# Performance work log

Hardware: AMD Instinct MI355X
Metric: run time of the kernel (lower is better)

The kernel has to match this reference:

```python
import jax, jax.numpy as jnp
import numpy as np

N = 50000
E = 800000
IN_DIM = 256
HID = 64
HEADS = 4
OUT_DIM = 40
NEG_SLOPE = 0.2


def _gatv2_conv(x, src, dst, Wl, bl, Wr, br, att, bias, concat):
    """PyG GATv2Conv (share_weights=False, eval mode, no attn dropout).
    src -> message source nodes, dst -> target nodes (softmax over dst)."""
    H, C = att.shape
    n = x.shape[0]
    xl = (x @ Wl + bl).reshape(n, H, C)  # source/message transform (lin_l)
    xr = (x @ Wr + br).reshape(n, H, C)  # target transform (lin_r)
    # per-edge logits: [E, H]
    s = xl[src] + xr[dst]                                  # [E,H,C]
    e = jnp.einsum('ehc,hc->eh', jax.nn.leaky_relu(s, NEG_SLOPE), att)
    # segment softmax over incoming edges of each target node
    m = jax.ops.segment_max(e, dst, num_segments=n)        # [N,H]
    m = jnp.where(jnp.isfinite(m), m, 0.0)                 # empty segments
    ex = jnp.exp(e - m[dst])
    denom = jax.ops.segment_sum(ex, dst, num_segments=n)   # [N,H]
    alpha = ex / (denom[dst] + 1e-16)                      # [E,H]
    out = jax.ops.segment_sum(alpha[:, :, None] * xl[src], dst, num_segments=n)
    if concat:
        out = out.reshape(n, H * C)
    else:
        out = out.mean(axis=1)
    return out + bias


def setup_inputs() -> dict:
    key = jax.random.key(0)
    ks = jax.random.split(key, 12)
    sc = 0.05
    return {
        'x': jax.random.normal(ks[0], (N, IN_DIM), jnp.float32),
        'src': jax.random.randint(ks[1], (E,), 0, N, jnp.int32),
        'dst': jax.random.randint(ks[2], (E,), 0, N, jnp.int32),
        'Wl1': jax.random.normal(ks[3], (IN_DIM, HEADS * HID), jnp.float32) * sc,
        'bl1': jnp.zeros((HEADS * HID,), jnp.float32),
        'Wr1': jax.random.normal(ks[4], (IN_DIM, HEADS * HID), jnp.float32) * sc,
        'br1': jnp.zeros((HEADS * HID,), jnp.float32),
        'att1': jax.random.normal(ks[5], (HEADS, HID), jnp.float32) * sc,
        'bias1': jnp.zeros((HEADS * HID,), jnp.float32),
        'Wl2': jax.random.normal(ks[6], (HEADS * HID, HEADS * HID), jnp.float32) * sc,
        'bl2': jnp.zeros((HEADS * HID,), jnp.float32),
        'Wr2': jax.random.normal(ks[7], (HEADS * HID, HEADS * HID), jnp.float32) * sc,
        'br2': jnp.zeros((HEADS * HID,), jnp.float32),
        'att2': jax.random.normal(ks[8], (HEADS, HID), jnp.float32) * sc,
        'bias2': jnp.zeros((HID,), jnp.float32),
        'Wc': jax.random.normal(ks[9], (HID, OUT_DIM), jnp.float32) * sc,
        'bc': jnp.zeros((OUT_DIM,), jnp.float32),
    }


def reference(x, src, dst, Wl1, bl1, Wr1, br1, att1, bias1,
              Wl2, bl2, Wr2, br2, att2, bias2, Wc, bc):
    h = _gatv2_conv(x, src, dst, Wl1, bl1, Wr1, br1, att1, bias1, concat=True)
    h = jax.nn.relu(h)  # dropout p applied only in training; eval -> identity
    h = _gatv2_conv(h, src, dst, Wl2, bl2, Wr2, br2, att2, bias2, concat=False)
    h = jax.nn.relu(h)
    return h @ Wc + bc  # [N, OUT_DIM]
```

## Files before the change

### kernel.cpp

```cpp
#include <hip/hip_runtime.h>
#include <hip/hip_bf16.h>
#include <math.h>


#define IN_DIM 256
#define HIDHC 256
#define HID 64
#define OUT_DIM 40

using half8  = __attribute__((ext_vector_type(8))) _Float16;
using half4  = __attribute__((ext_vector_type(4))) _Float16;
using half2v = __attribute__((ext_vector_type(2))) _Float16;
using f32x4  = __attribute__((ext_vector_type(4))) float;

__device__ __forceinline__ void gload16(const void* g, void* l) {
    __builtin_amdgcn_global_load_lds(
        (const __attribute__((address_space(1))) void*)g,
        (__attribute__((address_space(3))) void*)l, 16, 0, 0);
}


__global__ void edge_hist(const int* __restrict__ dst, int* __restrict__ deg, int E) {
    int i = blockIdx.x * blockDim.x + threadIdx.x;
    if (i < E) atomicAdd(&deg[dst[i]], 1);
}

__global__ void deg_block_reduce(const int* __restrict__ deg, int* __restrict__ bsum, int n) {
    int i = blockIdx.x * 256 + threadIdx.x;
    int v = (i < n) ? deg[i] : 0;
    #pragma unroll
    for (int off = 32; off; off >>= 1) v += __shfl_xor(v, off, 64);
    __shared__ int ws[4];
    int lane = threadIdx.x & 63, wid = threadIdx.x >> 6;
    if (lane == 0) ws[wid] = v;
    __syncthreads();
    if (threadIdx.x == 0) bsum[blockIdx.x] = ws[0] + ws[1] + ws[2] + ws[3];
}

__global__ void scan_bsums(const int* __restrict__ bsum, int* __restrict__ bpre, int nb) {
    __shared__ int s[256];
    int tid = threadIdx.x;
    int orig = (tid < nb) ? bsum[tid] : 0;
    s[tid] = orig;
    __syncthreads();
    #pragma unroll
    for (int off = 1; off < 256; off <<= 1) {
        int t = (tid >= off) ? s[tid - off] : 0;
        __syncthreads();
        s[tid] += t;
        __syncthreads();
    }
    if (tid < nb) bpre[tid] = s[tid] - orig;
}

__global__ void deg_scan_apply(const int* __restrict__ deg, const int* __restrict__ bpre,
                               int* __restrict__ offsets, int* __restrict__ cursor, int n) {
    int i = blockIdx.x * 256 + threadIdx.x;
    int lane = threadIdx.x & 63, wid = threadIdx.x >> 6;
    int v = (i < n) ? deg[i] : 0;
    int inc = v;
    #pragma unroll
    for (int off = 1; off < 64; off <<= 1) {
        int t = __shfl_up(inc, off, 64);
        if (lane >= off) inc += t;
    }
    __shared__ int ws[4];
    if (lane == 63) ws[wid] = inc;
    __syncthreads();
    int add = bpre[blockIdx.x];
    for (int w = 0; w < wid; ++w) add += ws[w];
    int incl = inc + add;
    if (i < n) { offsets[i + 1] = incl; cursor[i] = incl - v; }
    if (i == 0) offsets[0] = 0;
}

__global__ void edge_scatter(const int* __restrict__ src, const int* __restrict__ dst,
                             int* __restrict__ cursor, int* __restrict__ csr_src, int E) {
    int i = blockIdx.x * blockDim.x + threadIdx.x;
    if (i < E) {
        int p = atomicAdd(&cursor[dst[i]], 1);
        csr_src[p] = src[i];
    }
}


__global__ void cvt_f16(const float* __restrict__ in, _Float16* __restrict__ out, int n4) {
    int i = blockIdx.x * blockDim.x + threadIdx.x;
    if (i >= n4) return;
    float4 v = ((const float4*)in)[i];
    half4 h = { (_Float16)v.x, (_Float16)v.y, (_Float16)v.z, (_Float16)v.w };
    ((half4*)out)[i] = h;
}

__global__ void prep_weights(const float* __restrict__ W0, const float* __restrict__ W1,
                             const float* __restrict__ W2, const float* __restrict__ W3,
                             _Float16* __restrict__ T) {
    const float* Wsel = (blockIdx.y == 0) ? W0 : (blockIdx.y == 1) ? W1
                      : (blockIdx.y == 2) ? W2 : W3;
    int k = blockIdx.x, nn = threadIdx.x;
    float v = Wsel[k * 256 + nn];
    T[(size_t)blockIdx.y * 65536 + (size_t)nn * 256 + k] = (_Float16)v;
}


__global__ __launch_bounds__(256) void gemm2_mfma(
    const _Float16* __restrict__ A,
    const _Float16* __restrict__ W0, const float* __restrict__ b0, _Float16* __restrict__ C0,
    const _Float16* __restrict__ W1, const float* __restrict__ b1, _Float16* __restrict__ C1,
    int M)
{
    __shared__ __align__(16) _Float16 sA[2][4096], sB[2][4096];

    const _Float16* W   = blockIdx.z ? W1 : W0;
    const float*    bias= blockIdx.z ? b1 : b0;
    _Float16*       C   = blockIdx.z ? C1 : C0;

    int tid = threadIdx.x;
    int bm = blockIdx.x * 128;
    int bn = blockIdx.y * 128;

    int lane = tid & 63, w = tid >> 6;
    int r = lane & 15, q = lane >> 4;
    int m0 = (w >> 1) * 64, n0 = (w & 1) * 64;

    int arow[2], brow[2], kgo[2], lds[2];
    #pragma unroll
    for (int i = 0; i < 2; ++i) {
        int g = tid + 256 * i;
        kgo[i] = (g >> 7) * 8;
        int row = g & 127;
        arow[i] = min(bm + row, M - 1);
        brow[i] = bn + row;
        lds[i] = g * 8;
    }

    f32x4 acc[4][4];
    #pragma unroll
    for (int i = 0; i < 4; ++i)
        #pragma unroll
        for (int j = 0; j < 4; ++j) acc[i][j] = (f32x4)0.f;

    #pragma unroll
    for (int i = 0; i < 2; ++i) {
        gload16(A + (size_t)arow[i] * 256 + kgo[i], &sA[0][lds[i]]);
        gload16(W + (size_t)brow[i] * 256 + kgo[i], &sB[0][lds[i]]);
    }
    __builtin_amdgcn_s_waitcnt(0);
    __syncthreads();

    #pragma unroll 1
    for (int kt = 0; kt < 8; ++kt) {
        int buf = kt & 1;
        if (kt < 7) {
            int k0 = (kt + 1) * 32;
            #pragma unroll
            for (int i = 0; i < 2; ++i) {
                gload16(A + (size_t)arow[i] * 256 + k0 + kgo[i], &sA[buf ^ 1][lds[i]]);
                gload16(W + (size_t)brow[i] * 256 + k0 + kgo[i], &sB[buf ^ 1][lds[i]]);
            }
        }
        half8 a[4], b[4];
        #pragma unroll
        for (int i = 0; i < 4; ++i) {
            a[i] = *(const half8*)(&sA[buf][(q * 128 + m0 + i * 16 + r) * 8]);
            b[i] = *(const half8*)(&sB[buf][(q * 128 + n0 + i * 16 + r) * 8]);
        }
        #pragma unroll
        for (int i = 0; i < 4; ++i)
            #pragma unroll
            for (int j = 0; j < 4; ++j)
                acc[i][j] = __builtin_amdgcn_mfma_f32_16x16x32_f16(a[i], b[j], acc[i][j], 0, 0, 0);
        __builtin_amdgcn_s_waitcnt(0);
        __syncthreads();
    }

    float bv[4];
    #pragma unroll
    for (int j = 0; j < 4; ++j) bv[j] = bias[bn + n0 + j * 16 + r];
    #pragma unroll
    for (int i = 0; i < 4; ++i) {
        #pragma unroll
        for (int reg = 0; reg < 4; ++reg) {
            int row = bm + m0 + i * 16 + q * 4 + reg;
            if (row < M) {
                #pragma unroll
                for (int j = 0; j < 4; ++j)
                    C[(size_t)row * 256 + bn + n0 + j * 16 + r] =
                        (_Float16)(acc[i][j][reg] + bv[j]);
            }
        }
    }
}


__global__ __launch_bounds__(256) void gat_node(
    const _Float16* __restrict__ xl, const _Float16* __restrict__ xr,
    const float* __restrict__ att, const float* __restrict__ bias,
    const int* __restrict__ offsets, const int* __restrict__ csr_src,
    void* __restrict__ out0, int n, int mode)
{
    int wid = threadIdx.x >> 6;
    int node = (blockIdx.x << 2) + wid;
    if (node >= n) return;
    int lane = threadIdx.x & 63;
    int H = lane >> 5;
    int p = lane & 31;

    const half2v c02 = { (_Float16)0.2f, (_Float16)0.2f };

    half8 xrh = *(const half8*)(xr + (size_t)node * HIDHC + p * 8);
    half2v xr01 = __builtin_shufflevector(xrh, xrh, 0, 1);
    half2v xr23 = __builtin_shufflevector(xrh, xrh, 2, 3);
    half2v xr45 = __builtin_shufflevector(xrh, xrh, 4, 5);
    half2v xr67 = __builtin_shufflevector(xrh, xrh, 6, 7);

    float4 af0 = *(const float4*)(att + p * 8);
    float4 af1 = *(const float4*)(att + p * 8 + 4);
    half2v at01 = { (_Float16)af0.x, (_Float16)af0.y };
    half2v at23 = { (_Float16)af0.z, (_Float16)af0.w };
    half2v at45 = { (_Float16)af1.x, (_Float16)af1.y };
    half2v at67 = { (_Float16)af1.z, (_Float16)af1.w };

    float acc[8];
    #pragma unroll
    for (int k = 0; k < 8; ++k) acc[k] = 0.f;
    float d = 0.f;

    int j0 = __builtin_amdgcn_readfirstlane(offsets[node]);
    int j1 = __builtin_amdgcn_readfirstlane(offsets[node + 1]);

    int j = j0;
    for (; j + 2 <= j1; j += 2) {
        int s0 = __builtin_amdgcn_readfirstlane(csr_src[j]);
        int s1 = __builtin_amdgcn_readfirstlane(csr_src[j + 1]);
        int s = H ? s1 : s0;
        half8 h = *(const half8*)(xl + (size_t)s * HIDHC + p * 8);
        half2v h01 = __builtin_shufflevector(h, h, 0, 1);
        half2v h23 = __builtin_shufflevector(h, h, 2, 3);
        half2v h45 = __builtin_shufflevector(h, h, 4, 5);
        half2v h67 = __builtin_shufflevector(h, h, 6, 7);
        half2v s01 = h01 + xr01, s23 = h23 + xr23, s45 = h45 + xr45, s67 = h67 + xr67;
        half2v l01 = __builtin_elementwise_max(s01, s01 * c02);
        half2v l23 = __builtin_elementwise_max(s23, s23 * c02);
        half2v l45 = __builtin_elementwise_max(s45, s45 * c02);
        half2v l67 = __builtin_elementwise_max(s67, s67 * c02);
        float e = __builtin_amdgcn_fdot2(l01, at01, 0.f, false);
        e = __builtin_amdgcn_fdot2(l23, at23, e, false);
        e = __builtin_amdgcn_fdot2(l45, at45, e, false);
        e = __builtin_amdgcn_fdot2(l67, at67, e, false);
        e += __shfl_xor(e, 1);
        e += __shfl_xor(e, 2);
        e += __shfl_xor(e, 4);
        float pw = __expf(e);
        d += pw;
        #pragma unroll
        for (int k = 0; k < 8; ++k) acc[k] = fmaf(pw, (float)h[k], acc[k]);
    }
    if (j < j1) {
        int s0 = __builtin_amdgcn_readfirstlane(csr_src[j]);
        half8 h = *(const half8*)(xl + (size_t)s0 * HIDHC + p * 8);
        half2v h01 = __builtin_shufflevector(h, h, 0, 1);
        half2v h23 = __builtin_shufflevector(h, h, 2, 3);
        half2v h45 = __builtin_shufflevector(h, h, 4, 5);
        half2v h67 = __builtin_shufflevector(h, h, 6, 7);
        half2v s01 = h01 + xr01, s23 = h23 + xr23, s45 = h45 + xr45, s67 = h67 + xr67;
        half2v l01 = __builtin_elementwise_max(s01, s01 * c02);
        half2v l23 = __builtin_elementwise_max(s23, s23 * c02);
        half2v l45 = __builtin_elementwise_max(s45, s45 * c02);
        half2v l67 = __builtin_elementwise_max(s67, s67 * c02);
        float e = __builtin_amdgcn_fdot2(l01, at01, 0.f, false);
        e = __builtin_amdgcn_fdot2(l23, at23, e, false);
        e = __builtin_amdgcn_fdot2(l45, at45, e, false);
        e = __builtin_amdgcn_fdot2(l67, at67, e, false);
        e += __shfl_xor(e, 1);
        e += __shfl_xor(e, 2);
        e += __shfl_xor(e, 4);
        float pw = (H == 0) ? __expf(e) : 0.f;
        d += pw;
        #pragma unroll
        for (int k = 0; k < 8; ++k) acc[k] = fmaf(pw, (float)h[k], acc[k]);
    }

    d += __shfl_xor(d, 32);
    #pragma unroll
    for (int k = 0; k < 8; ++k) acc[k] += __shfl_xor(acc[k], 32);

    float inv = 1.f / (d + 1e-16f);
    float o[8];
    #pragma unroll
    for (int k = 0; k < 8; ++k) o[k] = acc[k] * inv;

    if (mode == 0) {
        if (H == 0) {
            float4 b0 = *(const float4*)(bias + p * 8);
            float4 b1 = *(const float4*)(bias + p * 8 + 4);
            float bb[8] = { b0.x, b0.y, b0.z, b0.w, b1.x, b1.y, b1.z, b1.w };
            half8 hh;
            #pragma unroll
            for (int k = 0; k < 8; ++k) hh[k] = (_Float16)fmaxf(o[k] + bb[k], 0.f);
            *(half8*)((_Float16*)out0 + (size_t)node * HIDHC + p * 8) = hh;
        }
    } else {
        #pragma unroll
        for (int k = 0; k < 8; ++k) {
            o[k] += __shfl_xor(o[k], 8);
            o[k] += __shfl_xor(o[k], 16);
        }
        if (lane < 8) {
            float4 b0 = *(const float4*)(bias + p * 8);
            float4 b1 = *(const float4*)(bias + p * 8 + 4);
            float bb[8] = { b0.x, b0.y, b0.z, b0.w, b1.x, b1.y, b1.z, b1.w };
            float4 o0, o1;
            o0.x = fmaxf(o[0] * 0.25f + bb[0], 0.f);
            o0.y = fmaxf(o[1] * 0.25f + bb[1], 0.f);
            o0.z = fmaxf(o[2] * 0.25f + bb[2], 0.f);
            o0.w = fmaxf(o[3] * 0.25f + bb[3], 0.f);
            o1.x = fmaxf(o[4] * 0.25f + bb[4], 0.f);
            o1.y = fmaxf(o[5] * 0.25f + bb[5], 0.f);
            o1.z = fmaxf(o[6] * 0.25f + bb[6], 0.f);
            o1.w = fmaxf(o[7] * 0.25f + bb[7], 0.f);
            float* dst = (float*)out0 + (size_t)node * HID + p * 8;
            *(float4*)dst = o0;
            *(float4*)(dst + 4) = o1;
        }
    }
}


__global__ __launch_bounds__(256) void final_linear(
    const float* __restrict__ h2, const float* __restrict__ Wc,
    const float* __restrict__ bc, float* __restrict__ out, int n)
{
    __shared__ float Ws[HID * OUT_DIM];
    __shared__ float bs[OUT_DIM];
    __shared__ float hs[64][HID + 1];

    for (int i = threadIdx.x; i < HID * OUT_DIM; i += 256) Ws[i] = Wc[i];
    if (threadIdx.x < OUT_DIM) bs[threadIdx.x] = bc[threadIdx.x];

    int n0 = blockIdx.x * 64;
    for (int i = threadIdx.x; i < 64 * HID; i += 256) {
        int r = i >> 6, c = i & 63;
        int node = n0 + r;
        hs[r][c] = (node < n) ? h2[(size_t)node * HID + c] : 0.f;
    }
    __syncthreads();

    for (int idx = threadIdx.x; idx < 64 * OUT_DIM; idx += 256) {
        int r = idx / OUT_DIM, o = idx % OUT_DIM;
        int node = n0 + r;
        if (node < n) {
            float s = bs[o];
            #pragma unroll
            for (int c = 0; c < HID; ++c) s = fmaf(hs[r][c], Ws[c * OUT_DIM + o], s);
            out[(size_t)node * OUT_DIM + o] = s;
        }
    }
}


extern "C" void kernel_launch(void* const* d_in, const int* in_sizes, int n_in,
                              void* d_out, int out_size, void* d_ws, size_t ws_size,
                              hipStream_t stream) {
    const int N = in_sizes[0] / IN_DIM;
    const int E = in_sizes[1];

    const float* x    = (const float*)d_in[0];
    const int*   src  = (const int*)d_in[1];
    const int*   dst  = (const int*)d_in[2];
    const float* Wl1  = (const float*)d_in[3];
    const float* bl1  = (const float*)d_in[4];
    const float* Wr1  = (const float*)d_in[5];
    const float* br1  = (const float*)d_in[6];
    const float* att1 = (const float*)d_in[7];
    const float* bias1= (const float*)d_in[8];
    const float* Wl2  = (const float*)d_in[9];
    const float* bl2  = (const float*)d_in[10];
    const float* Wr2  = (const float*)d_in[11];
    const float* br2  = (const float*)d_in[12];
    const float* att2 = (const float*)d_in[13];
    const float* bias2= (const float*)d_in[14];
    const float* Wc   = (const float*)d_in[15];
    const float* bc   = (const float*)d_in[16];

    char* ws = (char*)d_ws;
    size_t off = 0;
    _Float16* xlh = (_Float16*)(ws + off); off += (size_t)N * HIDHC * 2;
    _Float16* xrh = (_Float16*)(ws + off); off += (size_t)N * HIDHC * 2;
    _Float16* Af  = (_Float16*)(ws + off); off += (size_t)N * HIDHC * 2;
    float*    h2  = (float*)(ws + off);    off += (size_t)N * HID * 4;
    _Float16* Wt  = (_Float16*)(ws + off); off += (size_t)4 * 65536 * 2;
    int* deg     = (int*)(ws + off); off += (size_t)N * 4;
    int* offsets = (int*)(ws + off); off += (size_t)(N + 1) * 4;
    int* cursor  = (int*)(ws + off); off += (size_t)N * 4;
    int* csr     = (int*)(ws + off); off += (size_t)E * 4;
    int* bsum    = (int*)(ws + off); off += 256 * 4;
    int* bpre    = (int*)(ws + off); off += 256 * 4;

    const int NB = (N + 255) / 256;

    hipMemsetAsync(deg, 0, (size_t)N * 4, stream);
    edge_hist<<<(E + 255) / 256, 256, 0, stream>>>(dst, deg, E);
    deg_block_reduce<<<NB, 256, 0, stream>>>(deg, bsum, N);
    scan_bsums<<<1, 256, 0, stream>>>(bsum, bpre, NB);
    deg_scan_apply<<<NB, 256, 0, stream>>>(deg, bpre, offsets, cursor, N);
    edge_scatter<<<(E + 255) / 256, 256, 0, stream>>>(src, dst, cursor, csr, E);
    prep_weights<<<dim3(256, 4), 256, 0, stream>>>(Wl1, Wr1, Wl2, Wr2, Wt);
    cvt_f16<<<(N * HIDHC / 4 + 255) / 256, 256, 0, stream>>>(x, Af, N * HIDHC / 4);

    const int KW = 65536;
    dim3 gg((N + 127) / 128, 2, 2);
    gemm2_mfma<<<gg, 256, 0, stream>>>(Af,
        Wt + 0 * KW, bl1, xlh,
        Wt + 1 * KW, br1, xrh, N);
    gat_node<<<(N + 3) / 4, 256, 0, stream>>>(xlh, xrh, att1, bias1, offsets, csr,
                                              (void*)Af, N, 0);
    gemm2_mfma<<<gg, 256, 0, stream>>>(Af,
        Wt + 2 * KW, bl2, xlh,
        Wt + 3 * KW, br2, xrh, N);
    gat_node<<<(N + 3) / 4, 256, 0, stream>>>(xlh, xrh, att2, bias2, offsets, csr,
                                              (void*)h2, N, 1);
    final_linear<<<(N + 63) / 64, 256, 0, stream>>>(h2, Wc, bc, (float*)d_out, N);
}
```

Measured before the change: 457.5 us.

## Merge prep kernels, fuse edge scatter into GEMM launch, fuse final linear into GAT

Combines the fp16 conversion, weight transpose and degree histogram into one launch. It also runs the CSR edge scatter as extra blocks of the first GEMM launch, and folds the final 64x40 linear layer into the second GAT node kernel using Wc staged in shared memory and shuffle reductions. The aim is to cut launch count and avoid writing and re-reading the h2 intermediate. The cost is extra shared memory and a block-wide sync in every gat_node launch, which may lower occupancy. Scatter blocks also share the grid with GEMM blocks.

```diff
diff --git a/kernel.cpp b/kernel.cpp
--- a/kernel.cpp
+++ b/kernel.cpp
@@ -20,10 +20,37 @@
 }
 
 
-__global__ void edge_hist(const int* __restrict__ dst, int* __restrict__ deg, int E) {
-    int i = blockIdx.x * blockDim.x + threadIdx.x;
+__global__ __launch_bounds__(256) void prep_all(
+    const float* __restrict__ x, _Float16* __restrict__ Af, int n4,
+    const float* __restrict__ W0, const float* __restrict__ W1,
+    const float* __restrict__ W2, const float* __restrict__ W3,
+    _Float16* __restrict__ T,
+    const int* __restrict__ dst, int* __restrict__ deg, int E,
+    int nbCvt, int nbW)
+{
+    int b = blockIdx.x;
+    if (b < nbCvt) {
+        int i = b * 256 + threadIdx.x;
+        if (i < n4) {
+            float4 v = ((const float4*)x)[i];
+            half4 h = { (_Float16)v.x, (_Float16)v.y, (_Float16)v.z, (_Float16)v.w };
+            ((half4*)Af)[i] = h;
+        }
+        return;
+    }
+    if (b < nbCvt + nbW) {
+        int b2 = b - nbCvt;
+        int k = b2 & 255, w = b2 >> 8;
+        const float* Wsel = (w == 0) ? W0 : (w == 1) ? W1 : (w == 2) ? W2 : W3;
+        int nn = threadIdx.x;
+        float v = Wsel[k * 256 + nn];
+        T[(size_t)w * 65536 + (size_t)nn * 256 + k] = (_Float16)v;
+        return;
+    }
+    int i = (b - nbCvt - nbW) * 256 + threadIdx.x;
     if (i < E) atomicAdd(&deg[dst[i]], 1);
 }
+
 
 __global__ void deg_block_reduce(const int* __restrict__ deg, int* __restrict__ bsum, int n) {
     int i = blockIdx.x * 256 + threadIdx.x;
@@ -74,50 +101,38 @@
     if (i == 0) offsets[0] = 0;
 }
 
-__global__ void edge_scatter(const int* __restrict__ src, const int* __restrict__ dst,
-                             int* __restrict__ cursor, int* __restrict__ csr_src, int E) {
-    int i = blockIdx.x * blockDim.x + threadIdx.x;
-    if (i < E) {
-        int p = atomicAdd(&cursor[dst[i]], 1);
-        csr_src[p] = src[i];
-    }
-}
-
-
-__global__ void cvt_f16(const float* __restrict__ in, _Float16* __restrict__ out, int n4) {
-    int i = blockIdx.x * blockDim.x + threadIdx.x;
-    if (i >= n4) return;
-    float4 v = ((const float4*)in)[i];
-    half4 h = { (_Float16)v.x, (_Float16)v.y, (_Float16)v.z, (_Float16)v.w };
-    ((half4*)out)[i] = h;
-}
-
-__global__ void prep_weights(const float* __restrict__ W0, const float* __restrict__ W1,
-                             const float* __restrict__ W2, const float* __restrict__ W3,
-                             _Float16* __restrict__ T) {
-    const float* Wsel = (blockIdx.y == 0) ? W0 : (blockIdx.y == 1) ? W1
-                      : (blockIdx.y == 2) ? W2 : W3;
-    int k = blockIdx.x, nn = threadIdx.x;
-    float v = Wsel[k * 256 + nn];
-    T[(size_t)blockIdx.y * 65536 + (size_t)nn * 256 + k] = (_Float16)v;
-}
-
-
-__global__ __launch_bounds__(256) void gemm2_mfma(
+
+__global__ __launch_bounds__(256) void gemm_scatter(
     const _Float16* __restrict__ A,
     const _Float16* __restrict__ W0, const float* __restrict__ b0, _Float16* __restrict__ C0,
     const _Float16* __restrict__ W1, const float* __restrict__ b1, _Float16* __restrict__ C1,
-    int M)
+    int M, int Mb,
+    const int* __restrict__ src, const int* __restrict__ dstv,
+    int* __restrict__ cursor, int* __restrict__ csr, int E, int scatterBlocks)
 {
     __shared__ __align__(16) _Float16 sA[2][4096], sB[2][4096];
 
-    const _Float16* W   = blockIdx.z ? W1 : W0;
-    const float*    bias= blockIdx.z ? b1 : b0;
-    _Float16*       C   = blockIdx.z ? C1 : C0;
+    int blk = blockIdx.x;
+    if (blk < scatterBlocks) {
+        int i = blk * 256 + threadIdx.x;
+        if (i < E) {
+            int pos = atomicAdd(&cursor[dstv[i]], 1);
+            csr[pos] = src[i];
+        }
+        return;
+    }
+    int bb = blk - scatterBlocks;
+    int bx = bb % Mb;
+    int byz = bb / Mb;
+    int by = byz & 1, bz = byz >> 1;
+
+    const _Float16* W   = bz ? W1 : W0;
+    const float*    bias= bz ? b1 : b0;
+    _Float16*       C   = bz ? C1 : C0;
 
     int tid = threadIdx.x;
-    int bm = blockIdx.x * 128;
-    int bn = blockIdx.y * 128;
+    int bm = bx * 128;
+    int bn = by * 128;
 
     int lane = tid & 63, w = tid >> 6;
     int r = lane & 15, q = lane >> 4;
@@ -197,8 +212,17 @@
     const _Float16* __restrict__ xl, const _Float16* __restrict__ xr,
     const float* __restrict__ att, const float* __restrict__ bias,
     const int* __restrict__ offsets, const int* __restrict__ csr_src,
-    void* __restrict__ out0, int n, int mode)
+    void* __restrict__ out0, const float* __restrict__ Wc,
+    const float* __restrict__ bc, int n, int mode)
 {
+    __shared__ float sWc[HID * OUT_DIM];
+    __shared__ float sbc[OUT_DIM];
+    if (mode == 1) {
+        for (int i = threadIdx.x; i < HID * OUT_DIM; i += 256) sWc[i] = Wc[i];
+        if (threadIdx.x < OUT_DIM) sbc[threadIdx.x] = bc[threadIdx.x];
+        __syncthreads();
+    }
+
     int wid = threadIdx.x >> 6;
     int node = (blockIdx.x << 2) + wid;
     if (node >= n) return;
@@ -306,54 +330,32 @@
             o[k] += __shfl_xor(o[k], 8);
             o[k] += __shfl_xor(o[k], 16);
         }
-        if (lane < 8) {
-            float4 b0 = *(const float4*)(bias + p * 8);
-            float4 b1 = *(const float4*)(bias + p * 8 + 4);
-            float bb[8] = { b0.x, b0.y, b0.z, b0.w, b1.x, b1.y, b1.z, b1.w };
-            float4 o0, o1;
-            o0.x = fmaxf(o[0] * 0.25f + bb[0], 0.f);
-            o0.y = fmaxf(o[1] * 0.25f + bb[1], 0.f);
-            o0.z = fmaxf(o[2] * 0.25f + bb[2], 0.f);
-            o0.w = fmaxf(o[3] * 0.25f + bb[3], 0.f);
-            o1.x = fmaxf(o[4] * 0.25f + bb[4], 0.f);
-            o1.y = fmaxf(o[5] * 0.25f + bb[5], 0.f);
-            o1.z = fmaxf(o[6] * 0.25f + bb[6], 0.f);
-            o1.w = fmaxf(o[7] * 0.25f + bb[7], 0.f);
-            float* dst = (float*)out0 + (size_t)node * HID + p * 8;
-            *(float4*)dst = o0;
-            *(float4*)(dst + 4) = o1;
-        }
-    }
-}
-
-
-__global__ __launch_bounds__(256) void final_linear(
-    const float* __restrict__ h2, const float* __restrict__ Wc,
-    const float* __restrict__ bc, float* __restrict__ out, int n)
-{
-    __shared__ float Ws[HID * OUT_DIM];
-    __shared__ float bs[OUT_DIM];
-    __shared__ float hs[64][HID + 1];
-
-    for (int i = threadIdx.x; i < HID * OUT_DIM; i += 256) Ws[i] = Wc[i];
-    if (threadIdx.x < OUT_DIM) bs[threadIdx.x] = bc[threadIdx.x];
-
-    int n0 = blockIdx.x * 64;
-    for (int i = threadIdx.x; i < 64 * HID; i += 256) {
-        int r = i >> 6, c = i & 63;
-        int node = n0 + r;
-        hs[r][c] = (node < n) ? h2[(size_t)node * HID + c] : 0.f;
-    }
-    __syncthreads();
-
-    for (int idx = threadIdx.x; idx < 64 * OUT_DIM; idx += 256) {
-        int r = idx / OUT_DIM, o = idx % OUT_DIM;
-        int node = n0 + r;
-        if (node < n) {
-            float s = bs[o];
+        int c = lane & 7;
+        int g = lane >> 3;
+        float4 b0 = *(const float4*)(bias + c * 8);
+        float4 b1 = *(const float4*)(bias + c * 8 + 4);
+        float bb[8] = { b0.x, b0.y, b0.z, b0.w, b1.x, b1.y, b1.z, b1.w };
+        float h2v[8];
+        #pragma unroll
+        for (int k = 0; k < 8; ++k) h2v[k] = fmaxf(o[k] * 0.25f + bb[k], 0.f);
+        float partial[5];
+        #pragma unroll
+        for (int m = 0; m < 5; ++m) {
+            float s = 0.f;
             #pragma unroll
-            for (int c = 0; c < HID; ++c) s = fmaf(hs[r][c], Ws[c * OUT_DIM + o], s);
-            out[(size_t)node * OUT_DIM + o] = s;
+            for (int k = 0; k < 8; ++k)
+                s = fmaf(h2v[k], sWc[(c * 8 + k) * OUT_DIM + 5 * g + m], s);
+            partial[m] = s;
+        }
+        #pragma unroll
+        for (int m = 0; m < 5; ++m) {
+            partial[m] += __shfl_xor(partial[m], 1);
+            partial[m] += __shfl_xor(partial[m], 2);
+            partial[m] += __shfl_xor(partial[m], 4);
+        }
+        if (c < 5) {
+            int oidx = 5 * g + c;
+            ((float*)out0)[(size_t)node * OUT_DIM + oidx] = partial[c] + sbc[oidx];
         }
     }
 }
@@ -388,7 +390,6 @@
     _Float16* xlh = (_Float16*)(ws + off); off += (size_t)N * HIDHC * 2;
     _Float16* xrh = (_Float16*)(ws + off); off += (size_t)N * HIDHC * 2;
     _Float16* Af  = (_Float16*)(ws + off); off += (size_t)N * HIDHC * 2;
-    float*    h2  = (float*)(ws + off);    off += (size_t)N * HID * 4;
     _Float16* Wt  = (_Float16*)(ws + off); off += (size_t)4 * 65536 * 2;
     int* deg     = (int*)(ws + off); off += (size_t)N * 4;
     int* offsets = (int*)(ws + off); off += (size_t)(N + 1) * 4;
@@ -398,27 +399,27 @@
     int* bpre    = (int*)(ws + off); off += 256 * 4;
 
     const int NB = (N + 255) / 256;
+    const int n4 = N * HIDHC / 4;
+    const int nbCvt = (n4 + 255) / 256;
+    const int nbW = 1024;
+    const int nbE = (E + 255) / 256;
+    const int Mb = (N + 127) / 128;
+    const int KW = 65536;
 
     hipMemsetAsync(deg, 0, (size_t)N * 4, stream);
-    edge_hist<<<(E + 255) / 256, 256, 0, stream>>>(dst, deg, E);
+    prep_all<<<nbCvt + nbW + nbE, 256, 0, stream>>>(x, Af, n4,
+        Wl1, Wr1, Wl2, Wr2, Wt, dst, deg, E, nbCvt, nbW);
     deg_block_reduce<<<NB, 256, 0, stream>>>(deg, bsum, N);
     scan_bsums<<<1, 256, 0, stream>>>(bsum, bpre, NB);
     deg_scan_apply<<<NB, 256, 0, stream>>>(deg, bpre, offsets, cursor, N);
-    edge_scatter<<<(E + 255) / 256, 256, 0, stream>>>(src, dst, cursor, csr, E);
-    prep_weights<<<dim3(256, 4), 256, 0, stream>>>(Wl1, Wr1, Wl2, Wr2, Wt);
-    cvt_f16<<<(N * HIDHC / 4 + 255) / 256, 256, 0, stream>>>(x, Af, N * HIDHC / 4);
-
-    const int KW = 65536;
-    dim3 gg((N + 127) / 128, 2, 2);
-    gemm2_mfma<<<gg, 256, 0, stream>>>(Af,
-        Wt + 0 * KW, bl1, xlh,
-        Wt + 1 * KW, br1, xrh, N);
+    gemm_scatter<<<nbE + Mb * 4, 256, 0, stream>>>(Af,
+        Wt + 0 * KW, bl1, xlh, Wt + 1 * KW, br1, xrh, N, Mb,
+        src, dst, cursor, csr, E, nbE);
     gat_node<<<(N + 3) / 4, 256, 0, stream>>>(xlh, xrh, att1, bias1, offsets, csr,
-                                              (void*)Af, N, 0);
-    gemm2_mfma<<<gg, 256, 0, stream>>>(Af,
-        Wt + 2 * KW, bl2, xlh,
-        Wt + 3 * KW, br2, xrh, N);
+                                              (void*)Af, Wc, bc, N, 0);
+    gemm_scatter<<<Mb * 4, 256, 0, stream>>>(Af,
+        Wt + 2 * KW, bl2, xlh, Wt + 3 * KW, br2, xrh, N, Mb,
+        src, dst, cursor, csr, E, 0);
     gat_node<<<(N + 3) / 4, 256, 0, stream>>>(xlh, xrh, att2, bias2, offsets, csr,
-                                              (void*)h2, N, 1);
-    final_linear<<<(N + 63) / 64, 256, 0, stream>>>(h2, Wc, bc, (float*)d_out, N);
-}
+                                              d_out, Wc, bc, N, 1);
+}
```

New measurement: 474.8 us. 3.8% more time.
